# Kernel optimization log

Measured on AMD Instinct MI355X. Metric: run time of the kernel, lower is better.

## Reference

```python
import jax, jax.numpy as jnp
import numpy as np

# Maxwell rheological model constants (from init_kwargs)
E_INFTY = 1.0  # long-term equilibrium spring stiffness
E = 2.0        # Maxwell-branch spring stiffness
ETA = 1.0      # dashpot viscosity

B, T = 16384, 2048


def setup_inputs() -> dict:
    key = jax.random.key(0)
    k1, k2 = jax.random.split(key)
    strains = jax.random.normal(k1, (B, T), dtype=jnp.float32)
    # timestep sizes: positive, small
    dts = jax.random.uniform(k2, (B, T), dtype=jnp.float32)
    return {"strains": strains, "dts": dts}


def reference(strains, dts):
    # strains, dts: [B, T]. Recurrence runs over time axis; gamma[0]=sigma[0]=0.
    eps_t = strains.T  # [T, B]
    dt_t = dts.T       # [T, B]
    a = E / ETA

    def step(gamma, xs):
        eps_n, dt_n, eps_next = xs
        # explicit-Euler update of internal (viscous) strain
        gamma_new = gamma + dt_n * a * (eps_n - gamma)
        # stress at step n+1
        sigma = E_INFTY * eps_next + E * (eps_next - gamma_new)
        return gamma_new, sigma

    init = jnp.zeros_like(eps_t[0])  # gamma[0] = 0
    xs = (eps_t[:-1], dt_t[:-1], eps_t[1:])
    _, sigmas = jax.lax.scan(step, init, xs)  # sigmas: [T-1, B]
    zero_row = jnp.zeros((1, strains.shape[0]), strains.dtype)  # sigma[0] = 0
    stresses = jnp.concatenate([zero_row, sigmas], axis=0)  # [T, B]
    return stresses.T  # [B, T]
```

## Files before the change

kernel.cpp:

```cpp
#include <hip/hip_runtime.h>


#define T_LEN 2048

__global__ __launch_bounds__(256) void maxwell_scan_kernel(
    const float* __restrict__ eps_g, const float* __restrict__ dt_g,
    float* __restrict__ out_g)
{
    const int row = blockIdx.x;
    const int tid = threadIdx.x;
    const long base = (long)row * T_LEN + (long)tid * 8;

    const float4 e0 = *(const float4*)(eps_g + base);
    const float4 e1 = *(const float4*)(eps_g + base + 4);
    const float4 d0 = *(const float4*)(dt_g + base);
    const float4 d1 = *(const float4*)(dt_g + base + 4);

    float e[8] = {e0.x, e0.y, e0.z, e0.w, e1.x, e1.y, e1.z, e1.w};
    float d[8] = {d0.x, d0.y, d0.z, d0.w, d1.x, d1.y, d1.z, d1.w};

    float P = 1.0f, Q = 0.0f;
    #pragma unroll
    for (int k = 0; k < 8; ++k) {
        const float ad = 2.0f * d[k];
        const float A  = 1.0f - ad;
        const float Bv = ad * e[k];
        Q = A * Q + Bv;
        P = A * P;
    }

    const int lane = tid & 63;
    const int wid  = tid >> 6;
    #pragma unroll
    for (int dd = 1; dd < 64; dd <<= 1) {
        const float Pp = __shfl_up(P, dd);
        const float Qp = __shfl_up(Q, dd);
        if (lane >= dd) {
            Q = P * Qp + Q;
            P = P * Pp;
        }
    }

    __shared__ float sP[4], sQ[4];
    if (lane == 63) { sP[wid] = P; sQ[wid] = Q; }
    __syncthreads();

    float Qw = 0.0f;
    for (int w = 0; w < wid; ++w) {
        Qw = sP[w] * Qw + sQ[w];
    }

    float Pe = __shfl_up(P, 1);
    float Qe = __shfl_up(Q, 1);
    if (lane == 0) { Pe = 1.0f; Qe = 0.0f; }

    float g = Pe * Qw + Qe;

    float o[8];
    o[0] = 3.0f * e[0] - 2.0f * g;
    #pragma unroll
    for (int k = 1; k < 8; ++k) {
        g = g + 2.0f * d[k - 1] * (e[k - 1] - g);
        o[k] = 3.0f * e[k] - 2.0f * g;
    }
    if (tid == 0) o[0] = 0.0f;

    float4 w0 = make_float4(o[0], o[1], o[2], o[3]);
    float4 w1 = make_float4(o[4], o[5], o[6], o[7]);
    *(float4*)(out_g + base)     = w0;
    *(float4*)(out_g + base + 4) = w1;
}

extern "C" void kernel_launch(void* const* d_in, const int* in_sizes, int n_in,
                              void* d_out, int out_size, void* d_ws, size_t ws_size,
                              hipStream_t stream) {
    const float* strains = (const float*)d_in[0];
    const float* dts     = (const float*)d_in[1];
    float* out           = (float*)d_out;

    const int B = in_sizes[0] / T_LEN;
    maxwell_scan_kernel<<<B, 256, 0, stream>>>(strains, dts, out);
}
```

Before: 305.3 us.

## Map each row to one wavefront with 32 elements per lane

Replaces the one-row-per-block scan with one row per 64-lane wavefront, each lane handling 32 contiguous elements. This removes the shared-memory cross-wave combine and the block barrier. The block now processes four rows. In exchange, per-lane register use and the serial dependency chain grow, and the strided per-lane float4 accesses may be less coalesced per instruction.

Measured after the change: 324.6 us. +6.3%, slower.

```diff
diff --git a/kernel.cpp b/kernel.cpp
--- a/kernel.cpp
+++ b/kernel.cpp
@@ -2,73 +2,62 @@
 
 
 #define T_LEN 2048
+#define EPT 32
+#define ROWS_PER_BLOCK 4
 
-__global__ __launch_bounds__(256) void maxwell_scan_kernel(
+__global__ __launch_bounds__(256) void maxwell_wave_kernel(
     const float* __restrict__ eps_g, const float* __restrict__ dt_g,
-    float* __restrict__ out_g)
+    float* __restrict__ out_g, int nrows)
 {
-    const int row = blockIdx.x;
-    const int tid = threadIdx.x;
-    const long base = (long)row * T_LEN + (long)tid * 8;
+    const int lane = threadIdx.x & 63;
+    const int w    = threadIdx.x >> 6;
+    const long row = (long)blockIdx.x * ROWS_PER_BLOCK + w;
+    if (row >= nrows) return;
+    const long base = row * T_LEN + (long)lane * EPT;
 
-    const float4 e0 = *(const float4*)(eps_g + base);
-    const float4 e1 = *(const float4*)(eps_g + base + 4);
-    const float4 d0 = *(const float4*)(dt_g + base);
-    const float4 d1 = *(const float4*)(dt_g + base + 4);
-
-    float e[8] = {e0.x, e0.y, e0.z, e0.w, e1.x, e1.y, e1.z, e1.w};
-    float d[8] = {d0.x, d0.y, d0.z, d0.w, d1.x, d1.y, d1.z, d1.w};
+    float e[EPT], d[EPT];
+    #pragma unroll
+    for (int i = 0; i < EPT / 4; ++i) {
+        const float4 v = *(const float4*)(eps_g + base + i * 4);
+        e[4*i+0] = v.x; e[4*i+1] = v.y; e[4*i+2] = v.z; e[4*i+3] = v.w;
+    }
+    #pragma unroll
+    for (int i = 0; i < EPT / 4; ++i) {
+        const float4 v = *(const float4*)(dt_g + base + i * 4);
+        d[4*i+0] = v.x; d[4*i+1] = v.y; d[4*i+2] = v.z; d[4*i+3] = v.w;
+    }
 
     float P = 1.0f, Q = 0.0f;
     #pragma unroll
-    for (int k = 0; k < 8; ++k) {
+    for (int k = 0; k < EPT; ++k) {
         const float ad = 2.0f * d[k];
         const float A  = 1.0f - ad;
-        const float Bv = ad * e[k];
-        Q = A * Q + Bv;
-        P = A * P;
+        Q = fmaf(A, Q, ad * e[k]);
+        P *= A;
     }
 
-    const int lane = tid & 63;
-    const int wid  = tid >> 6;
     #pragma unroll
     for (int dd = 1; dd < 64; dd <<= 1) {
         const float Pp = __shfl_up(P, dd);
         const float Qp = __shfl_up(Q, dd);
-        if (lane >= dd) {
-            Q = P * Qp + Q;
-            P = P * Pp;
-        }
+        if (lane >= dd) { Q = fmaf(P, Qp, Q); P *= Pp; }
     }
 
-    __shared__ float sP[4], sQ[4];
-    if (lane == 63) { sP[wid] = P; sQ[wid] = Q; }
-    __syncthreads();
+    float g = __shfl_up(Q, 1);
+    if (lane == 0) g = 0.0f;
 
-    float Qw = 0.0f;
-    for (int w = 0; w < wid; ++w) {
-        Qw = sP[w] * Qw + sQ[w];
+    #pragma unroll
+    for (int i = 0; i < EPT / 4; ++i) {
+        float o[4];
+        #pragma unroll
+        for (int j = 0; j < 4; ++j) {
+            const int k = 4 * i + j;
+            o[j] = fmaf(3.0f, e[k], -2.0f * g);
+            g = fmaf(2.0f * d[k], e[k] - g, g);
+        }
+        if (lane == 0 && i == 0) o[0] = 0.0f;
+        *(float4*)(out_g + base + i * 4) = make_float4(o[0], o[1], o[2], o[3]);
     }
-
-    float Pe = __shfl_up(P, 1);
-    float Qe = __shfl_up(Q, 1);
-    if (lane == 0) { Pe = 1.0f; Qe = 0.0f; }
-
-    float g = Pe * Qw + Qe;
-
-    float o[8];
-    o[0] = 3.0f * e[0] - 2.0f * g;
-    #pragma unroll
-    for (int k = 1; k < 8; ++k) {
-        g = g + 2.0f * d[k - 1] * (e[k - 1] - g);
-        o[k] = 3.0f * e[k] - 2.0f * g;
-    }
-    if (tid == 0) o[0] = 0.0f;
-
-    float4 w0 = make_float4(o[0], o[1], o[2], o[3]);
-    float4 w1 = make_float4(o[4], o[5], o[6], o[7]);
-    *(float4*)(out_g + base)     = w0;
-    *(float4*)(out_g + base + 4) = w1;
 }
 
 extern "C" void kernel_launch(void* const* d_in, const int* in_sizes, int n_in,
@@ -78,6 +67,7 @@
     const float* dts     = (const float*)d_in[1];
     float* out           = (float*)d_out;
 
-    const int B = in_sizes[0] / T_LEN;
-    maxwell_scan_kernel<<<B, 256, 0, stream>>>(strains, dts, out);
+    const int nrows  = in_sizes[0] / T_LEN;
+    const int blocks = (nrows + ROWS_PER_BLOCK - 1) / ROWS_PER_BLOCK;
+    maxwell_wave_kernel<<<blocks, 256, 0, stream>>>(strains, dts, out, nrows);
 }
```

## Process four rows per block with two-row interleave and prefetch pipeline

Applied to the files above, without the earlier changes.

Each block now handles four rows, scanning two rows at a time so the two independent scans interleave for ILP. The loads for the next row pair are issued before the current pair is computed, and outputs use nontemporal stores. The goal is to hide memory latency and cut per-block launch overhead in a memory-bound kernel. In exchange it raises register pressure, and nrows must be divisible by four.

Result: slower. 325.9 us (+6.7%).

```diff
diff --git a/kernel.cpp b/kernel.cpp
--- a/kernel.cpp
+++ b/kernel.cpp
@@ -1,74 +1,115 @@
 #include <hip/hip_runtime.h>
 
 
+typedef float v4f __attribute__((ext_vector_type(4)));
+
 #define T_LEN 2048
+#define RPB 4
 
-__global__ __launch_bounds__(256) void maxwell_scan_kernel(
+__global__ __launch_bounds__(256) void maxwell_pipe_kernel(
     const float* __restrict__ eps_g, const float* __restrict__ dt_g,
-    float* __restrict__ out_g)
+    float* __restrict__ out_g, int nrows)
 {
-    const int row = blockIdx.x;
-    const int tid = threadIdx.x;
-    const long base = (long)row * T_LEN + (long)tid * 8;
+    const int tid  = threadIdx.x;
+    const int lane = tid & 63;
+    const int wid  = tid >> 6;
+    const long row0 = (long)blockIdx.x * RPB;
+    const long tb   = (long)tid * 8;
 
-    const float4 e0 = *(const float4*)(eps_g + base);
-    const float4 e1 = *(const float4*)(eps_g + base + 4);
-    const float4 d0 = *(const float4*)(dt_g + base);
-    const float4 d1 = *(const float4*)(dt_g + base + 4);
+    __shared__ float sP[2][2][4], sQ[2][2][4];
 
-    float e[8] = {e0.x, e0.y, e0.z, e0.w, e1.x, e1.y, e1.z, e1.w};
-    float d[8] = {d0.x, d0.y, d0.z, d0.w, d1.x, d1.y, d1.z, d1.w};
-
-    float P = 1.0f, Q = 0.0f;
-    #pragma unroll
-    for (int k = 0; k < 8; ++k) {
-        const float ad = 2.0f * d[k];
-        const float A  = 1.0f - ad;
-        const float Bv = ad * e[k];
-        Q = A * Q + Bv;
-        P = A * P;
+    v4f eA0, eA1, dA0, dA1, eB0, eB1, dB0, dB1;
+    {
+        const float* pA = eps_g + row0 * T_LEN + tb;
+        const float* qA = dt_g  + row0 * T_LEN + tb;
+        eA0 = *(const v4f*)pA;           eA1 = *(const v4f*)(pA + 4);
+        eB0 = *(const v4f*)(pA + T_LEN); eB1 = *(const v4f*)(pA + T_LEN + 4);
+        dA0 = *(const v4f*)qA;           dA1 = *(const v4f*)(qA + 4);
+        dB0 = *(const v4f*)(qA + T_LEN); dB1 = *(const v4f*)(qA + T_LEN + 4);
     }
 
-    const int lane = tid & 63;
-    const int wid  = tid >> 6;
     #pragma unroll
-    for (int dd = 1; dd < 64; dd <<= 1) {
-        const float Pp = __shfl_up(P, dd);
-        const float Qp = __shfl_up(Q, dd);
-        if (lane >= dd) {
-            Q = P * Qp + Q;
-            P = P * Pp;
+    for (int it = 0; it < RPB / 2; ++it) {
+        const long rA = row0 + 2 * it;
+
+        v4f neA0, neA1, ndA0, ndA1, neB0, neB1, ndB0, ndB1;
+        if (it + 1 < RPB / 2) {
+            const float* pA = eps_g + (rA + 2) * T_LEN + tb;
+            const float* qA = dt_g  + (rA + 2) * T_LEN + tb;
+            neA0 = *(const v4f*)pA;           neA1 = *(const v4f*)(pA + 4);
+            neB0 = *(const v4f*)(pA + T_LEN); neB1 = *(const v4f*)(pA + T_LEN + 4);
+            ndA0 = *(const v4f*)qA;           ndA1 = *(const v4f*)(qA + 4);
+            ndB0 = *(const v4f*)(qA + T_LEN); ndB1 = *(const v4f*)(qA + T_LEN + 4);
+        }
+
+        float eA[8] = {eA0.x,eA0.y,eA0.z,eA0.w, eA1.x,eA1.y,eA1.z,eA1.w};
+        float dA[8] = {dA0.x,dA0.y,dA0.z,dA0.w, dA1.x,dA1.y,dA1.z,dA1.w};
+        float eB[8] = {eB0.x,eB0.y,eB0.z,eB0.w, eB1.x,eB1.y,eB1.z,eB1.w};
+        float dB[8] = {dB0.x,dB0.y,dB0.z,dB0.w, dB1.x,dB1.y,dB1.z,dB1.w};
+
+        float PA = 1.0f, QA = 0.0f, PB = 1.0f, QB = 0.0f;
+        #pragma unroll
+        for (int k = 0; k < 8; ++k) {
+            const float adA = 2.0f * dA[k];
+            const float adB = 2.0f * dB[k];
+            QA = fmaf(1.0f - adA, QA, adA * eA[k]);  PA *= (1.0f - adA);
+            QB = fmaf(1.0f - adB, QB, adB * eB[k]);  PB *= (1.0f - adB);
+        }
+
+        #pragma unroll
+        for (int dd = 1; dd < 64; dd <<= 1) {
+            const float PpA = __shfl_up(PA, dd), QpA = __shfl_up(QA, dd);
+            const float PpB = __shfl_up(PB, dd), QpB = __shfl_up(QB, dd);
+            if (lane >= dd) {
+                QA = fmaf(PA, QpA, QA);  PA *= PpA;
+                QB = fmaf(PB, QpB, QB);  PB *= PpB;
+            }
+        }
+
+        if (lane == 63) {
+            sP[it & 1][0][wid] = PA;  sQ[it & 1][0][wid] = QA;
+            sP[it & 1][1][wid] = PB;  sQ[it & 1][1][wid] = QB;
+        }
+        __syncthreads();
+        float QwA = 0.0f, QwB = 0.0f;
+        for (int w = 0; w < wid; ++w) {
+            QwA = fmaf(sP[it & 1][0][w], QwA, sQ[it & 1][0][w]);
+            QwB = fmaf(sP[it & 1][1][w], QwB, sQ[it & 1][1][w]);
+        }
+
+        float PeA = __shfl_up(PA, 1), QeA = __shfl_up(QA, 1);
+        float PeB = __shfl_up(PB, 1), QeB = __shfl_up(QB, 1);
+        if (lane == 0) { PeA = 1.0f; QeA = 0.0f; PeB = 1.0f; QeB = 0.0f; }
+        float gA = fmaf(PeA, QwA, QeA);
+        float gB = fmaf(PeB, QwB, QeB);
+
+        float oA[8], oB[8];
+        oA[0] = fmaf(3.0f, eA[0], -2.0f * gA);
+        oB[0] = fmaf(3.0f, eB[0], -2.0f * gB);
+        #pragma unroll
+        for (int k = 1; k < 8; ++k) {
+            gA = fmaf(2.0f * dA[k-1], eA[k-1] - gA, gA);
+            gB = fmaf(2.0f * dB[k-1], eB[k-1] - gB, gB);
+            oA[k] = fmaf(3.0f, eA[k], -2.0f * gA);
+            oB[k] = fmaf(3.0f, eB[k], -2.0f * gB);
+        }
+        if (tid == 0) { oA[0] = 0.0f; oB[0] = 0.0f; }
+
+        float* outA = out_g + rA * T_LEN + tb;
+        v4f wA0 = {oA[0], oA[1], oA[2], oA[3]};
+        v4f wA1 = {oA[4], oA[5], oA[6], oA[7]};
+        v4f wB0 = {oB[0], oB[1], oB[2], oB[3]};
+        v4f wB1 = {oB[4], oB[5], oB[6], oB[7]};
+        __builtin_nontemporal_store(wA0, (v4f*)outA);
+        __builtin_nontemporal_store(wA1, (v4f*)(outA + 4));
+        __builtin_nontemporal_store(wB0, (v4f*)(outA + T_LEN));
+        __builtin_nontemporal_store(wB1, (v4f*)(outA + T_LEN + 4));
+
+        if (it + 1 < RPB / 2) {
+            eA0 = neA0; eA1 = neA1; dA0 = ndA0; dA1 = ndA1;
+            eB0 = neB0; eB1 = neB1; dB0 = ndB0; dB1 = ndB1;
         }
     }
-
-    __shared__ float sP[4], sQ[4];
-    if (lane == 63) { sP[wid] = P; sQ[wid] = Q; }
-    __syncthreads();
-
-    float Qw = 0.0f;
-    for (int w = 0; w < wid; ++w) {
-        Qw = sP[w] * Qw + sQ[w];
-    }
-
-    float Pe = __shfl_up(P, 1);
-    float Qe = __shfl_up(Q, 1);
-    if (lane == 0) { Pe = 1.0f; Qe = 0.0f; }
-
-    float g = Pe * Qw + Qe;
-
-    float o[8];
-    o[0] = 3.0f * e[0] - 2.0f * g;
-    #pragma unroll
-    for (int k = 1; k < 8; ++k) {
-        g = g + 2.0f * d[k - 1] * (e[k - 1] - g);
-        o[k] = 3.0f * e[k] - 2.0f * g;
-    }
-    if (tid == 0) o[0] = 0.0f;
-
-    float4 w0 = make_float4(o[0], o[1], o[2], o[3]);
-    float4 w1 = make_float4(o[4], o[5], o[6], o[7]);
-    *(float4*)(out_g + base)     = w0;
-    *(float4*)(out_g + base + 4) = w1;
 }
 
 extern "C" void kernel_launch(void* const* d_in, const int* in_sizes, int n_in,
@@ -78,6 +119,7 @@
     const float* dts     = (const float*)d_in[1];
     float* out           = (float*)d_out;
 
-    const int B = in_sizes[0] / T_LEN;
-    maxwell_scan_kernel<<<B, 256, 0, stream>>>(strains, dts, out);
+    const int nrows  = in_sizes[0] / T_LEN;
+    const int blocks = nrows / RPB;
+    maxwell_pipe_kernel<<<blocks, 256, 0, stream>>>(strains, dts, out, nrows);
 }
```
